# Kernel optimization log

Measured on AMD Instinct MI355X. Metric: run time of the kernel, lower is better.

## Reference

```python
import jax, jax.numpy as jnp
import numpy as np

T = 16          # timesteps
BATCH = 8       # video clips -> leading dim of x is BATCH*T = 128
C_IN = 768      # fixed by nn.Conv2d(768, redu_dim, 1)
D = 256         # redu_dim
K = 64          # num_centers
H = W = 28
EPS = 1e-12     # torch F.normalize eps


def _conv(x, w, padding):
    # x: [N,C,H,W], w: [O,I,kh,kw]
    return jax.lax.conv_general_dilated(
        x, w, window_strides=(1, 1), padding=padding,
        dimension_numbers=('NCHW', 'OIHW', 'NCHW'))


def setup_inputs() -> dict:
    key = jax.random.key(0)
    ks = jax.random.split(key, 9)
    x = jax.random.normal(ks[0], (BATCH * T, C_IN, H, W), dtype=jnp.float32)
    redu_w = jax.random.normal(ks[1], (D, C_IN, 1, 1), jnp.float32) * 0.02
    redu_b = jnp.zeros((D,), jnp.float32)
    share_w = jax.random.normal(ks[2], (K, D, 1, 1), jnp.float32) * 0.05
    share_b = jnp.zeros((K,), jnp.float32)
    U_z = jax.random.normal(ks[3], (K, K, 3, 3), jnp.float32) * 0.04
    U_r = jax.random.normal(ks[4], (K, K, 3, 3), jnp.float32) * 0.04
    U_h = jax.random.normal(ks[5], (K, K, 3, 3), jnp.float32) * 0.04
    centers = jax.random.normal(ks[6], (K, D), jnp.float32) * 0.06
    return {"x": x, "redu_w": redu_w, "redu_b": redu_b,
            "share_w": share_w, "share_b": share_b,
            "U_z": U_z, "U_r": U_r, "U_h": U_h,
            "centers": centers, "timesteps": T}


def reference(x, redu_w, redu_b, share_w, share_b, U_z, U_r, U_h, centers, timesteps):
    t = timesteps
    bt, _, h, w = x.shape
    b = bt // t
    k = share_w.shape[0]
    d = redu_w.shape[0]

    # channel reduction (1x1 conv)
    xr = _conv(x, redu_w, 'VALID') + redu_b[None, :, None, None]        # [bt,d,h,w]
    # shared assignment logits (1x1 conv)
    wxb = _conv(xr, share_w, 'VALID') + share_b[None, :, None, None]     # [bt,k,h,w]
    wxb = wxb.reshape(b, t, k, h, w).transpose(1, 0, 2, 3, 4)            # [t,b,k,h,w]

    # sequential ConvGRU over timesteps
    h0 = jnp.zeros((b, k, h, w), x.dtype)
    def step(h_tm1, w_t):
        z = jax.nn.sigmoid(w_t + _conv(h_tm1, U_z, 'SAME'))
        r = jax.nn.sigmoid(w_t + _conv(h_tm1, U_r, 'SAME'))
        hh = jnp.tanh(w_t + _conv(r * h_tm1, U_h, 'SAME'))
        h_new = (1.0 - z) * hh + z * h_tm1
        return h_new, h_new
    _, hs = jax.lax.scan(step, h0, wxb)                                  # [t,b,k,h,w]

    assign = hs.transpose(1, 0, 2, 3, 4).reshape(b * t, k, h * w)        # [bt,k,hw]
    # softmax over centers per spatial location
    assign = jax.nn.softmax(assign, axis=1)

    # VLAD aggregation
    a_sum = assign.sum(axis=-1, keepdims=True)                           # [bt,k,1]
    a = a_sum * centers[None]                                            # [bt,k,d]
    xf = xr.reshape(b * t, d, h * w)                                     # [bt,d,hw]
    vlad = jnp.einsum('bkp,bdp->bkd', assign, xf) - a                    # [bt,k,d]

    vlad = vlad.reshape(b, t, k, d).sum(axis=1)                          # [b,k,d]
    # intra-norm over feature dim, then global L2 norm
    vlad = vlad / jnp.maximum(jnp.linalg.norm(vlad, axis=2, keepdims=True), EPS)
    vlad = vlad.reshape(b, k * d)
    vlad = vlad / jnp.maximum(jnp.linalg.norm(vlad, axis=1, keepdims=True), EPS)
    return vlad
```

## Files before the change

kernel.cpp:

```cpp
#include <hip/hip_runtime.h>
#include <hip/hip_bf16.h>

#define T_ 16
#define B_ 8
#define CIN 768
#define D_ 256
#define K_ 64
#define HW 784
#define W_ 28

typedef short short8 __attribute__((ext_vector_type(8)));
typedef short short4v __attribute__((ext_vector_type(4)));
typedef float floatx4 __attribute__((ext_vector_type(4)));
typedef unsigned short ushort_t;

__device__ __forceinline__ unsigned short f2bf(float x) {
    union { float f; unsigned u; } v; v.f = x;
    unsigned u = v.u;
    unsigned r = (u + 0x7fffu + ((u >> 16) & 1u)) >> 16;
    return (unsigned short)r;
}
__device__ __forceinline__ float bf2f(unsigned short h) {
    union { unsigned u; float f; } v; v.u = ((unsigned)h) << 16; return v.f;
}

__device__ __forceinline__ float block_reduce_sum_256(float v) {
    for (int off = 32; off > 0; off >>= 1) v += __shfl_down(v, off, 64);
    __shared__ float red[4];
    __shared__ float tot;
    int lane = threadIdx.x & 63, wid = threadIdx.x >> 6;
    if (lane == 0) red[wid] = v;
    __syncthreads();
    if (threadIdx.x == 0) tot = red[0] + red[1] + red[2] + red[3];
    __syncthreads();
    return tot;
}

__global__ __launch_bounds__(256) void cvt_weights(
    const float* __restrict__ rw, const float* __restrict__ sw,
    const float* __restrict__ Uz, const float* __restrict__ Ur,
    const float* __restrict__ Uh,
    ushort_t* __restrict__ whi, ushort_t* __restrict__ wlo,
    ushort_t* __restrict__ shi, ushort_t* __restrict__ slo,
    ushort_t* __restrict__ azh, ushort_t* __restrict__ azl,
    ushort_t* __restrict__ ahh, ushort_t* __restrict__ ahl)
{
    int i = blockIdx.x * 256 + threadIdx.x;
    const int nR = D_ * CIN;
    const int nS = K_ * D_;
    const int nZR = 128 * 576;
    const int nH = 64 * 576;
    if (i < nR) {
        float x = rw[i];
        unsigned short h = f2bf(x);
        whi[i] = h; wlo[i] = f2bf(x - bf2f(h));
    } else if (i < nR + nS) {
        int j = i - nR;
        float x = sw[j];
        unsigned short h = f2bf(x);
        shi[j] = h; slo[j] = f2bf(x - bf2f(h));
    } else if (i < nR + nS + nZR) {
        int j = i - nR - nS;
        int row = j / 576, kk = j - row * 576;
        int tap = kk >> 6, c = kk & 63;
        const float* U = (row < 64) ? Uz : Ur;
        float x = U[(((size_t)(row & 63)) * 64 + c) * 9 + tap];
        unsigned short h = f2bf(x);
        azh[j] = h; azl[j] = f2bf(x - bf2f(h));
    } else if (i < nR + nS + nZR + nH) {
        int j = i - nR - nS - nZR;
        int row = j / 576, kk = j - row * 576;
        int tap = kk >> 6, c = kk & 63;
        float x = Uh[(((size_t)row) * 64 + c) * 9 + tap];
        unsigned short h = f2bf(x);
        ahh[j] = h; ahl[j] = f2bf(x - bf2f(h));
    }
}

template<int BM>
__global__ __launch_bounds__(256, 2) void mfma_conv1x1(
    const float* __restrict__ X, const ushort_t* __restrict__ Whi,
    const ushort_t* __restrict__ Wlo, const float* __restrict__ bias,
    float* __restrict__ Out, int Kdim)
{
    const int nt = blockIdx.x, bt = blockIdx.z;
    const int p0 = nt * 112;
    const int tid = threadIdx.x, lane = tid & 63, wv = tid >> 6;
    const float* Xb = X + (size_t)bt * Kdim * HW;
    float* Ob = Out + (size_t)bt * BM * HW;

    __shared__ ushort_t lA[2][BM * 40];
    __shared__ ushort_t lB[2][112 * 40];

    constexpr int NI = (BM == 256) ? 7 : 2;
    floatx4 acc[4][NI];
#pragma unroll
    for (int a = 0; a < 4; ++a)
#pragma unroll
        for (int b = 0; b < NI; ++b) acc[a][b] = (floatx4){0.f, 0.f, 0.f, 0.f};

    const int NKS = Kdim / 32;
    for (int ks = 0; ks < NKS; ++ks) {
        const int k0 = ks * 32;
#pragma unroll
        for (int i = 0; i < BM / 64; ++i) {
            int ch = tid + i * 256;
            int m = ch >> 2, j = ch & 3;
            uint4 hv = *(const uint4*)(Whi + (size_t)m * Kdim + k0 + j * 8);
            uint4 lv = *(const uint4*)(Wlo + (size_t)m * Kdim + k0 + j * 8);
            *(uint4*)&lA[0][m * 40 + j * 8] = hv;
            *(uint4*)&lA[1][m * 40 + j * 8] = lv;
        }
#pragma unroll
        for (int i = 0; i < 14; ++i) {
            int e = tid + i * 256;
            int cc = e / 112, pp = e - cc * 112;
            float xv = Xb[(size_t)(k0 + cc) * HW + p0 + pp];
            unsigned short h = f2bf(xv);
            lB[0][pp * 40 + cc] = h;
            lB[1][pp * 40 + cc] = f2bf(xv - bf2f(h));
        }
        __syncthreads();

        short8 ahi[4], alo[4];
        const int mbase = (BM == 256) ? wv * 64 : 0;
        const int koff = (lane >> 4) * 8;
#pragma unroll
        for (int mi = 0; mi < 4; ++mi) {
            int m = mbase + mi * 16 + (lane & 15);
            ahi[mi] = *(const short8*)&lA[0][m * 40 + koff];
            alo[mi] = *(const short8*)&lA[1][m * 40 + koff];
        }
        if constexpr (BM == 256) {
#pragma unroll
            for (int ni = 0; ni < 7; ++ni) {
                int n = ni * 16 + (lane & 15);
                short8 bhi = *(const short8*)&lB[0][n * 40 + koff];
                short8 blo = *(const short8*)&lB[1][n * 40 + koff];
#pragma unroll
                for (int mi = 0; mi < 4; ++mi) {
                    acc[mi][ni] = __builtin_amdgcn_mfma_f32_16x16x32_bf16(ahi[mi], bhi, acc[mi][ni], 0, 0, 0);
                    acc[mi][ni] = __builtin_amdgcn_mfma_f32_16x16x32_bf16(ahi[mi], blo, acc[mi][ni], 0, 0, 0);
                    acc[mi][ni] = __builtin_amdgcn_mfma_f32_16x16x32_bf16(alo[mi], bhi, acc[mi][ni], 0, 0, 0);
                }
            }
        } else {
#pragma unroll
            for (int nj = 0; nj < 2; ++nj) {
                int ni = wv * 2 + nj;
                if (ni >= 7) break;
                int n = ni * 16 + (lane & 15);
                short8 bhi = *(const short8*)&lB[0][n * 40 + koff];
                short8 blo = *(const short8*)&lB[1][n * 40 + koff];
#pragma unroll
                for (int mi = 0; mi < 4; ++mi) {
                    acc[mi][nj] = __builtin_amdgcn_mfma_f32_16x16x32_bf16(ahi[mi], bhi, acc[mi][nj], 0, 0, 0);
                    acc[mi][nj] = __builtin_amdgcn_mfma_f32_16x16x32_bf16(ahi[mi], blo, acc[mi][nj], 0, 0, 0);
                    acc[mi][nj] = __builtin_amdgcn_mfma_f32_16x16x32_bf16(alo[mi], bhi, acc[mi][nj], 0, 0, 0);
                }
            }
        }
        __syncthreads();
    }

    if constexpr (BM == 256) {
#pragma unroll
        for (int mi = 0; mi < 4; ++mi) {
            int m0g = wv * 64 + mi * 16 + ((lane >> 4) << 2);
#pragma unroll
            for (int ni = 0; ni < 7; ++ni) {
                int p = p0 + ni * 16 + (lane & 15);
#pragma unroll
                for (int r = 0; r < 4; ++r)
                    Ob[(size_t)(m0g + r) * HW + p] = acc[mi][ni][r] + bias[m0g + r];
            }
        }
    } else {
#pragma unroll
        for (int nj = 0; nj < 2; ++nj) {
            int ni = wv * 2 + nj;
            if (ni >= 7) break;
            int p = p0 + ni * 16 + (lane & 15);
#pragma unroll
            for (int mi = 0; mi < 4; ++mi) {
                int m0g = mi * 16 + ((lane >> 4) << 2);
#pragma unroll
                for (int r = 0; r < 4; ++r)
                    Ob[(size_t)(m0g + r) * HW + p] = acc[mi][nj][r] + bias[m0g + r];
            }
        }
    }
}

__device__ __forceinline__ void stage_tile(
    const ushort_t* __restrict__ ghi, const ushort_t* __restrict__ glo,
    ushort_t* Bhi, ushort_t* Blo, int y0, int tid)
{
    for (int e = tid; e < 6 * 30 * 8; e += 256) {
        int r = e / 240, rem = e - r * 240;
        int lx = rem >> 3, j = rem & 7;
        int gy = y0 - 1 + r, gx = lx - 1;
        short8 vh = {0, 0, 0, 0, 0, 0, 0, 0};
        short8 vl = {0, 0, 0, 0, 0, 0, 0, 0};
        if (gy >= 0 && gy < 28 && gx >= 0 && gx < 28) {
            size_t go = ((size_t)(gy * 28 + gx)) * 64 + j * 8;
            vh = *(const short8*)(ghi + go);
            vl = *(const short8*)(glo + go);
        }
        int lo = (r * 30 + lx) * 72 + j * 8;
        *(short8*)&Bhi[lo] = vh;
        *(short8*)&Blo[lo] = vl;
    }
}

__device__ __forceinline__ void gru_gemm(
    const ushort_t* __restrict__ Ahi, const ushort_t* __restrict__ Alo,
    int arow, int Astride,
    const ushort_t* Bhi, const ushort_t* Blo, int lane, floatx4 acc[7])
{
    const int koff8 = (lane >> 4) * 8;
    const int li = lane & 15;
    int yb[7], xb[7];
#pragma unroll
    for (int nf = 0; nf < 7; ++nf) {
        int pp = nf * 16 + li;
        yb[nf] = pp / 28; xb[nf] = pp - yb[nf] * 28;
    }
    for (int tap = 0; tap < 9; ++tap) {
        int dy = tap / 3, dx = tap - dy * 3;
#pragma unroll
        for (int ch = 0; ch < 2; ++ch) {
            int kk = tap * 64 + ch * 32 + koff8;
            short8 ahi = *(const short8*)(Ahi + (size_t)arow * Astride + kk);
            short8 alo = *(const short8*)(Alo + (size_t)arow * Astride + kk);
            int cbase = ch * 32 + koff8;
#pragma unroll
            for (int nf = 0; nf < 7; ++nf) {
                int o = ((yb[nf] + dy) * 30 + xb[nf] + dx) * 72 + cbase;
                short8 bhi = *(const short8*)&Bhi[o];
                short8 blo = *(const short8*)&Blo[o];
                acc[nf] = __builtin_amdgcn_mfma_f32_16x16x32_bf16(ahi, bhi, acc[nf], 0, 0, 0);
                acc[nf] = __builtin_amdgcn_mfma_f32_16x16x32_bf16(ahi, blo, acc[nf], 0, 0, 0);
                acc[nf] = __builtin_amdgcn_mfma_f32_16x16x32_bf16(alo, bhi, acc[nf], 0, 0, 0);
            }
        }
    }
}

__global__ __launch_bounds__(256, 2) void gru_zr_mfma(
    const ushort_t* __restrict__ hhi, const ushort_t* __restrict__ hlo,
    const ushort_t* __restrict__ azh, const ushort_t* __restrict__ azl,
    const float* __restrict__ wxb, const float* __restrict__ hprev_f,
    float* __restrict__ zbuf, ushort_t* __restrict__ rhi, ushort_t* __restrict__ rlo,
    int t)
{
    int rt = blockIdx.x, b = blockIdx.y, half = blockIdx.z;
    int y0 = rt * 4;
    int tid = threadIdx.x, lane = tid & 63, wv = tid >> 6;

    __shared__ ushort_t Bhi[6 * 30 * 72];
    __shared__ ushort_t Blo[6 * 30 * 72];
    stage_tile(hhi + (size_t)b * HW * 64, hlo + (size_t)b * HW * 64, Bhi, Blo, y0, tid);
    __syncthreads();

    floatx4 acc[7];
#pragma unroll
    for (int nf = 0; nf < 7; ++nf) acc[nf] = (floatx4){0.f, 0.f, 0.f, 0.f};

    int arow = half * 64 + wv * 16 + (lane & 15);
    gru_gemm(azh, azl, arow, 576, Bhi, Blo, lane, acc);

    int kbase = wv * 16 + ((lane >> 4) << 2);
    const float* wx = wxb + (((size_t)b * T_ + t) * K_) * HW;
    const float* hp = hprev_f + (size_t)b * K_ * HW;
#pragma unroll
    for (int nf = 0; nf < 7; ++nf) {
        int p = y0 * 28 + nf * 16 + (lane & 15);
        if (half == 0) {
#pragma unroll
            for (int r = 0; r < 4; ++r) {
                int k = kbase + r;
                float g = 1.f / (1.f + __expf(-(wx[(size_t)k * HW + p] + acc[nf][r])));
                zbuf[((size_t)b * K_ + k) * HW + p] = g;
            }
        } else {
            short4v vh, vl;
#pragma unroll
            for (int r = 0; r < 4; ++r) {
                int k = kbase + r;
                float g = 1.f / (1.f + __expf(-(wx[(size_t)k * HW + p] + acc[nf][r])));
                float rh = g * hp[(size_t)k * HW + p];
                unsigned short h = f2bf(rh);
                vh[r] = h; vl[r] = f2bf(rh - bf2f(h));
            }
            size_t o = (size_t)(b * HW + p) * 64 + kbase;
            *(short4v*)(rhi + o) = vh;
            *(short4v*)(rlo + o) = vl;
        }
    }
}

__global__ __launch_bounds__(256, 2) void gru_h_mfma(
    const ushort_t* __restrict__ rhi, const ushort_t* __restrict__ rlo,
    const ushort_t* __restrict__ ahh, const ushort_t* __restrict__ ahl,
    const float* __restrict__ wxb, const float* __restrict__ hprev_f,
    const float* __restrict__ zbuf, float* __restrict__ hs_t,
    ushort_t* __restrict__ hhi, ushort_t* __restrict__ hlo, int t)
{
    int rt = blockIdx.x, b = blockIdx.y;
    int y0 = rt * 4;
    int tid = threadIdx.x, lane = tid & 63, wv = tid >> 6;

    __shared__ ushort_t Bhi[6 * 30 * 72];
    __shared__ ushort_t Blo[6 * 30 * 72];
    stage_tile(rhi + (size_t)b * HW * 64, rlo + (size_t)b * HW * 64, Bhi, Blo, y0, tid);
    __syncthreads();

    floatx4 acc[7];
#pragma unroll
    for (int nf = 0; nf < 7; ++nf) acc[nf] = (floatx4){0.f, 0.f, 0.f, 0.f};

    int arow = wv * 16 + (lane & 15);
    gru_gemm(ahh, ahl, arow, 576, Bhi, Blo, lane, acc);

    int kbase = wv * 16 + ((lane >> 4) << 2);
    const float* wx = wxb + (((size_t)b * T_ + t) * K_) * HW;
    const float* hp = hprev_f + (size_t)b * K_ * HW;
#pragma unroll
    for (int nf = 0; nf < 7; ++nf) {
        int p = y0 * 28 + nf * 16 + (lane & 15);
        short4v vh, vl;
#pragma unroll
        for (int r = 0; r < 4; ++r) {
            int k = kbase + r;
            float xv = wx[(size_t)k * HW + p] + acc[nf][r];
            float e2 = __expf(2.f * xv);
            float th = 1.f - 2.f / (e2 + 1.f);
            float z = zbuf[((size_t)b * K_ + k) * HW + p];
            float hpv = hp[(size_t)k * HW + p];
            float hn = (1.f - z) * th + z * hpv;
            hs_t[((size_t)b * K_ + k) * HW + p] = hn;
            unsigned short h = f2bf(hn);
            vh[r] = h; vl[r] = f2bf(hn - bf2f(h));
        }
        size_t o = (size_t)(b * HW + p) * 64 + kbase;
        *(short4v*)(hhi + o) = vh;
        *(short4v*)(hlo + o) = vl;
    }
}

__global__ __launch_bounds__(256) void softmax_k(float* __restrict__ hs)
{
    int q = blockIdx.x;
    float* base = hs + (size_t)q * K_ * HW;
    for (int p = threadIdx.x; p < HW; p += 256) {
        float v[64];
        float m = -1e30f;
#pragma unroll
        for (int k = 0; k < 64; ++k) {
            v[k] = base[(size_t)k * HW + p];
            m = fmaxf(m, v[k]);
        }
        float s = 0.f;
#pragma unroll
        for (int k = 0; k < 64; ++k) {
            v[k] = __expf(v[k] - m);
            s += v[k];
        }
        float inv = 1.f / s;
#pragma unroll
        for (int k = 0; k < 64; ++k)
            base[(size_t)k * HW + p] = v[k] * inv;
    }
}

__global__ __launch_bounds__(256) void asum_k(const float* __restrict__ hs,
                                              float* __restrict__ asum)
{
    int bid = blockIdx.x; int b = bid >> 6, k = bid & 63;
    float s = 0.f;
    for (int t = 0; t < T_; ++t) {
        const float* row = hs + (((size_t)t * B_ + b) * K_ + k) * HW;
        for (int p = threadIdx.x; p < HW; p += 256) s += row[p];
    }
    float tot = block_reduce_sum_256(s);
    if (threadIdx.x == 0) asum[bid] = tot;
}

__global__ __launch_bounds__(256) void vlad_k(const float* __restrict__ assign,
    const float* __restrict__ xr, float* __restrict__ vladt)
{
    int dt = blockIdx.x, t = blockIdx.y, b = blockIdx.z;
    int q = t * B_ + b, bt = b * T_ + t, d0 = dt * 64;
    const float* ab = assign + (size_t)q * K_ * HW;
    const float* xb = xr + (size_t)bt * D_ * HW;
    __shared__ float As[16][68];
    __shared__ float Xs[16][68];
    int tx = threadIdx.x & 15, ty = threadIdx.x >> 4;
    float acc[4][4] = {{0.f}};

    for (int p0 = 0; p0 < HW; p0 += 16) {
#pragma unroll
        for (int it = 0; it < 4; ++it) {
            int e = threadIdx.x + it * 256;
            int row = e >> 4, pp = e & 15;
            As[pp][row] = ab[(size_t)row * HW + p0 + pp];
            Xs[pp][row] = xb[(size_t)(d0 + row) * HW + p0 + pp];
        }
        __syncthreads();
#pragma unroll
        for (int pp = 0; pp < 16; ++pp) {
            float4 a = *(const float4*)&As[pp][ty * 4];
            float4 xv = *(const float4*)&Xs[pp][tx * 4];
            float av[4] = {a.x, a.y, a.z, a.w};
            float xvv[4] = {xv.x, xv.y, xv.z, xv.w};
#pragma unroll
            for (int r = 0; r < 4; ++r)
#pragma unroll
                for (int s = 0; s < 4; ++s)
                    acc[r][s] = fmaf(av[r], xvv[s], acc[r][s]);
        }
        __syncthreads();
    }
#pragma unroll
    for (int r = 0; r < 4; ++r) {
        int k = ty * 4 + r;
        float4 o = {acc[r][0], acc[r][1], acc[r][2], acc[r][3]};
        *(float4*)&vladt[((size_t)bt * K_ + k) * D_ + d0 + tx * 4] = o;
    }
}

__global__ __launch_bounds__(256) void norm1_k(const float* __restrict__ vladt,
    const float* __restrict__ asum, const float* __restrict__ centers,
    float* __restrict__ out)
{
    int bid = blockIdx.x; int b = bid >> 6, k = bid & 63; int d = threadIdx.x;
    float acc = 0.f;
#pragma unroll
    for (int t = 0; t < T_; ++t)
        acc += vladt[(((size_t)b * T_ + t) * K_ + k) * D_ + d];
    acc -= asum[bid] * centers[(size_t)k * D_ + d];
    float ss = block_reduce_sum_256(acc * acc);
    float n = fmaxf(sqrtf(ss), 1e-12f);
    out[((size_t)b * K_ + k) * D_ + d] = acc / n;
}

__global__ __launch_bounds__(256) void norm2_k(float* __restrict__ out)
{
    int b = blockIdx.x;
    float* v = out + (size_t)b * (K_ * D_);
    float s = 0.f;
    for (int i = threadIdx.x; i < K_ * D_; i += 256) {
        float x = v[i];
        s = fmaf(x, x, s);
    }
    float tot = block_reduce_sum_256(s);
    float n = fmaxf(sqrtf(tot), 1e-12f);
    for (int i = threadIdx.x; i < K_ * D_; i += 256) v[i] = v[i] / n;
}

extern "C" void kernel_launch(void* const* d_in, const int* in_sizes, int n_in,
                              void* d_out, int out_size, void* d_ws, size_t ws_size,
                              hipStream_t stream)
{
    const float* x       = (const float*)d_in[0];
    const float* redu_w  = (const float*)d_in[1];
    const float* redu_b  = (const float*)d_in[2];
    const float* share_w = (const float*)d_in[3];
    const float* share_b = (const float*)d_in[4];
    const float* Uz      = (const float*)d_in[5];
    const float* Ur      = (const float*)d_in[6];
    const float* Uh      = (const float*)d_in[7];
    const float* centers = (const float*)d_in[8];

    float* ws = (float*)d_ws;
    const size_t SZ_XR   = (size_t)128 * D_ * HW;
    const size_t SZ_WXB  = (size_t)128 * K_ * HW;
    const size_t SZ_HS   = (size_t)T_ * B_ * K_ * HW;
    const size_t SZ_PLANE= (size_t)B_ * K_ * HW;

    float* xr    = ws;
    float* wxb   = xr + SZ_XR;
    float* hs    = wxb + SZ_WXB;
    float* h0    = hs + SZ_HS;
    float* zbuf  = h0 + SZ_PLANE;
    float* asumb = zbuf + SZ_PLANE;
    float* wsplit= asumb + 512;
    float* area  = wsplit + 323584;

    ushort_t* whi = (ushort_t*)wsplit;
    ushort_t* wlo = whi + 196608;
    ushort_t* shi = wlo + 196608;
    ushort_t* slo = shi + 16384;
    ushort_t* azh = slo + 16384;
    ushort_t* azl = azh + 73728;
    ushort_t* ahh = azl + 73728;
    ushort_t* ahl = ahh + 36864;

    float* vladt = area;
    ushort_t* hhi = (ushort_t*)area;
    ushort_t* hlo = hhi + SZ_PLANE;
    ushort_t* rhi = hlo + SZ_PLANE;
    ushort_t* rlo = rhi + SZ_PLANE;

    hipMemsetAsync(h0, 0, SZ_PLANE * sizeof(float), stream);
    hipMemsetAsync(hhi, 0, 2 * SZ_PLANE * sizeof(ushort_t), stream);

    cvt_weights<<<dim3((D_ * CIN + K_ * D_ + 128 * 576 + 64 * 576 + 255) / 256),
                  256, 0, stream>>>(redu_w, share_w, Uz, Ur, Uh,
                                    whi, wlo, shi, slo, azh, azl, ahh, ahl);

    mfma_conv1x1<256><<<dim3(7, 1, 128), 256, 0, stream>>>(x, whi, wlo, redu_b, xr, CIN);
    mfma_conv1x1<64><<<dim3(7, 1, 128), 256, 0, stream>>>(xr, shi, slo, share_b, wxb, D_);

    for (int t = 0; t < T_; ++t) {
        const float* hp = (t == 0) ? h0 : hs + (size_t)(t - 1) * SZ_PLANE;
        gru_zr_mfma<<<dim3(7, 8, 2), 256, 0, stream>>>(hhi, hlo, azh, azl, wxb, hp,
                                                       zbuf, rhi, rlo, t);
        gru_h_mfma<<<dim3(7, 8), 256, 0, stream>>>(rhi, rlo, ahh, ahl, wxb, hp, zbuf,
                                                   hs + (size_t)t * SZ_PLANE, hhi, hlo, t);
    }

    softmax_k<<<128, 256, 0, stream>>>(hs);
    asum_k<<<512, 256, 0, stream>>>(hs, asumb);

    vlad_k<<<dim3(4, 16, 8), 256, 0, stream>>>(hs, xr, vladt);
    norm1_k<<<512, 256, 0, stream>>>(vladt, asumb, centers, (float*)d_out);
    norm2_k<<<8, 256, 0, stream>>>((float*)d_out);
}
```

Before: 795.5 us.

## Fuse GRU gate kernels per step, pipeline conv1x1 loads, split softmax grid

```diff
diff --git a/kernel.cpp b/kernel.cpp
--- a/kernel.cpp
+++ b/kernel.cpp
@@ -77,64 +77,81 @@
     }
 }
 
-template<int BM>
+template<int BM, int KD>
 __global__ __launch_bounds__(256, 2) void mfma_conv1x1(
     const float* __restrict__ X, const ushort_t* __restrict__ Whi,
     const ushort_t* __restrict__ Wlo, const float* __restrict__ bias,
-    float* __restrict__ Out, int Kdim)
+    float* __restrict__ Out)
 {
     const int nt = blockIdx.x, bt = blockIdx.z;
     const int p0 = nt * 112;
     const int tid = threadIdx.x, lane = tid & 63, wv = tid >> 6;
-    const float* Xb = X + (size_t)bt * Kdim * HW;
+    const float* Xb = X + (size_t)bt * KD * HW;
     float* Ob = Out + (size_t)bt * BM * HW;
 
-    __shared__ ushort_t lA[2][BM * 40];
     __shared__ ushort_t lB[2][112 * 40];
 
     constexpr int NI = (BM == 256) ? 7 : 2;
+    constexpr int NKS = KD / 32;
     floatx4 acc[4][NI];
 #pragma unroll
     for (int a = 0; a < 4; ++a)
 #pragma unroll
         for (int b = 0; b < NI; ++b) acc[a][b] = (floatx4){0.f, 0.f, 0.f, 0.f};
 
-    const int NKS = Kdim / 32;
-    for (int ks = 0; ks < NKS; ++ks) {
-        const int k0 = ks * 32;
-#pragma unroll
-        for (int i = 0; i < BM / 64; ++i) {
-            int ch = tid + i * 256;
-            int m = ch >> 2, j = ch & 3;
-            uint4 hv = *(const uint4*)(Whi + (size_t)m * Kdim + k0 + j * 8);
-            uint4 lv = *(const uint4*)(Wlo + (size_t)m * Kdim + k0 + j * 8);
-            *(uint4*)&lA[0][m * 40 + j * 8] = hv;
-            *(uint4*)&lA[1][m * 40 + j * 8] = lv;
-        }
-#pragma unroll
-        for (int i = 0; i < 14; ++i) {
-            int e = tid + i * 256;
-            int cc = e / 112, pp = e - cc * 112;
-            float xv = Xb[(size_t)(k0 + cc) * HW + p0 + pp];
-            unsigned short h = f2bf(xv);
-            lB[0][pp * 40 + cc] = h;
-            lB[1][pp * 40 + cc] = f2bf(xv - bf2f(h));
-        }
-        __syncthreads();
-
-        short8 ahi[4], alo[4];
-        const int mbase = (BM == 256) ? wv * 64 : 0;
-        const int koff = (lane >> 4) * 8;
+    const int koff = (lane >> 4) * 8;
+    const int li = lane & 15;
+    const int mbase = (BM == 256) ? wv * 64 : 0;
+
+    const int u0j = tid / 112, u0p = tid - u0j * 112;
+    const bool u1v = tid < 192;
+    const int u1j = (tid + 256) / 112, u1p = (tid + 256) - u1j * 112;
+
+    float b0[16], b1[16];
+    short8 ahi[4], alo[4];
+
+    auto loadB = [&](int k0, float* bb) {
+        const float* xp0 = Xb + (size_t)(k0 + u0j * 8) * HW + p0 + u0p;
+#pragma unroll
+        for (int c = 0; c < 8; ++c) bb[c] = xp0[c * HW];
+        if (u1v) {
+            const float* xp1 = Xb + (size_t)(k0 + u1j * 8) * HW + p0 + u1p;
+#pragma unroll
+            for (int c = 0; c < 8; ++c) bb[8 + c] = xp1[c * HW];
+        }
+    };
+    auto writeB = [&](const float* bb) {
+        short8 vh, vl;
+#pragma unroll
+        for (int c = 0; c < 8; ++c) {
+            unsigned short h = f2bf(bb[c]);
+            vh[c] = (short)h; vl[c] = (short)f2bf(bb[c] - bf2f(h));
+        }
+        *(short8*)&lB[0][u0p * 40 + u0j * 8] = vh;
+        *(short8*)&lB[1][u0p * 40 + u0j * 8] = vl;
+        if (u1v) {
+#pragma unroll
+            for (int c = 0; c < 8; ++c) {
+                unsigned short h = f2bf(bb[8 + c]);
+                vh[c] = (short)h; vl[c] = (short)f2bf(bb[8 + c] - bf2f(h));
+            }
+            *(short8*)&lB[0][u1p * 40 + u1j * 8] = vh;
+            *(short8*)&lB[1][u1p * 40 + u1j * 8] = vl;
+        }
+    };
+    auto loadA = [&](int k0) {
 #pragma unroll
         for (int mi = 0; mi < 4; ++mi) {
-            int m = mbase + mi * 16 + (lane & 15);
-            ahi[mi] = *(const short8*)&lA[0][m * 40 + koff];
-            alo[mi] = *(const short8*)&lA[1][m * 40 + koff];
-        }
+            int m = mbase + mi * 16 + li;
+            ahi[mi] = *(const short8*)(Whi + (size_t)m * KD + k0 + koff);
+            alo[mi] = *(const short8*)(Wlo + (size_t)m * KD + k0 + koff);
+        }
+    };
+    auto domfma = [&]() {
         if constexpr (BM == 256) {
 #pragma unroll
             for (int ni = 0; ni < 7; ++ni) {
-                int n = ni * 16 + (lane & 15);
+                int n = ni * 16 + li;
                 short8 bhi = *(const short8*)&lB[0][n * 40 + koff];
                 short8 blo = *(const short8*)&lB[1][n * 40 + koff];
 #pragma unroll
@@ -149,7 +166,7 @@
             for (int nj = 0; nj < 2; ++nj) {
                 int ni = wv * 2 + nj;
                 if (ni >= 7) break;
-                int n = ni * 16 + (lane & 15);
+                int n = ni * 16 + li;
                 short8 bhi = *(const short8*)&lB[0][n * 40 + koff];
                 short8 blo = *(const short8*)&lB[1][n * 40 + koff];
 #pragma unroll
@@ -160,6 +177,21 @@
                 }
             }
         }
+    };
+
+    loadB(0, b0);
+    for (int ks = 0; ks < NKS; ks += 2) {
+        loadA(ks * 32);
+        writeB(b0);
+        __syncthreads();
+        if (ks + 1 < NKS) loadB((ks + 1) * 32, b1);
+        domfma();
+        __syncthreads();
+        loadA((ks + 1) * 32);
+        writeB(b1);
+        __syncthreads();
+        if (ks + 2 < NKS) loadB((ks + 2) * 32, b0);
+        domfma();
         __syncthreads();
     }
 
@@ -169,7 +201,7 @@
             int m0g = wv * 64 + mi * 16 + ((lane >> 4) << 2);
 #pragma unroll
             for (int ni = 0; ni < 7; ++ni) {
-                int p = p0 + ni * 16 + (lane & 15);
+                int p = p0 + ni * 16 + li;
 #pragma unroll
                 for (int r = 0; r < 4; ++r)
                     Ob[(size_t)(m0g + r) * HW + p] = acc[mi][ni][r] + bias[m0g + r];
@@ -180,7 +212,7 @@
         for (int nj = 0; nj < 2; ++nj) {
             int ni = wv * 2 + nj;
             if (ni >= 7) break;
-            int p = p0 + ni * 16 + (lane & 15);
+            int p = p0 + ni * 16 + li;
 #pragma unroll
             for (int mi = 0; mi < 4; ++mi) {
                 int m0g = mi * 16 + ((lane >> 4) << 2);
@@ -192,168 +224,216 @@
     }
 }
 
-__device__ __forceinline__ void stage_tile(
-    const ushort_t* __restrict__ ghi, const ushort_t* __restrict__ glo,
-    ushort_t* Bhi, ushort_t* Blo, int y0, int tid)
-{
-    for (int e = tid; e < 6 * 30 * 8; e += 256) {
-        int r = e / 240, rem = e - r * 240;
-        int lx = rem >> 3, j = rem & 7;
-        int gy = y0 - 1 + r, gx = lx - 1;
-        short8 vh = {0, 0, 0, 0, 0, 0, 0, 0};
-        short8 vl = {0, 0, 0, 0, 0, 0, 0, 0};
-        if (gy >= 0 && gy < 28 && gx >= 0 && gx < 28) {
-            size_t go = ((size_t)(gy * 28 + gx)) * 64 + j * 8;
-            vh = *(const short8*)(ghi + go);
-            vl = *(const short8*)(glo + go);
-        }
-        int lo = (r * 30 + lx) * 72 + j * 8;
-        *(short8*)&Bhi[lo] = vh;
-        *(short8*)&Blo[lo] = vl;
-    }
-}
-
-__device__ __forceinline__ void gru_gemm(
-    const ushort_t* __restrict__ Ahi, const ushort_t* __restrict__ Alo,
-    int arow, int Astride,
-    const ushort_t* Bhi, const ushort_t* Blo, int lane, floatx4 acc[7])
-{
-    const int koff8 = (lane >> 4) * 8;
-    const int li = lane & 15;
-    int yb[7], xb[7];
-#pragma unroll
-    for (int nf = 0; nf < 7; ++nf) {
-        int pp = nf * 16 + li;
-        yb[nf] = pp / 28; xb[nf] = pp - yb[nf] * 28;
-    }
-    for (int tap = 0; tap < 9; ++tap) {
-        int dy = tap / 3, dx = tap - dy * 3;
-#pragma unroll
-        for (int ch = 0; ch < 2; ++ch) {
-            int kk = tap * 64 + ch * 32 + koff8;
-            short8 ahi = *(const short8*)(Ahi + (size_t)arow * Astride + kk);
-            short8 alo = *(const short8*)(Alo + (size_t)arow * Astride + kk);
-            int cbase = ch * 32 + koff8;
-#pragma unroll
-            for (int nf = 0; nf < 7; ++nf) {
-                int o = ((yb[nf] + dy) * 30 + xb[nf] + dx) * 72 + cbase;
-                short8 bhi = *(const short8*)&Bhi[o];
-                short8 blo = *(const short8*)&Blo[o];
-                acc[nf] = __builtin_amdgcn_mfma_f32_16x16x32_bf16(ahi, bhi, acc[nf], 0, 0, 0);
-                acc[nf] = __builtin_amdgcn_mfma_f32_16x16x32_bf16(ahi, blo, acc[nf], 0, 0, 0);
-                acc[nf] = __builtin_amdgcn_mfma_f32_16x16x32_bf16(alo, bhi, acc[nf], 0, 0, 0);
-            }
-        }
-    }
-}
-
-__global__ __launch_bounds__(256, 2) void gru_zr_mfma(
-    const ushort_t* __restrict__ hhi, const ushort_t* __restrict__ hlo,
+__global__ __launch_bounds__(512, 2) void gru_step(
+    const ushort_t* __restrict__ hRhi, const ushort_t* __restrict__ hRlo,
+    ushort_t* __restrict__ hWhi, ushort_t* __restrict__ hWlo,
     const ushort_t* __restrict__ azh, const ushort_t* __restrict__ azl,
-    const float* __restrict__ wxb, const float* __restrict__ hprev_f,
-    float* __restrict__ zbuf, ushort_t* __restrict__ rhi, ushort_t* __restrict__ rlo,
-    int t)
-{
-    int rt = blockIdx.x, b = blockIdx.y, half = blockIdx.z;
-    int y0 = rt * 4;
-    int tid = threadIdx.x, lane = tid & 63, wv = tid >> 6;
-
-    __shared__ ushort_t Bhi[6 * 30 * 72];
-    __shared__ ushort_t Blo[6 * 30 * 72];
-    stage_tile(hhi + (size_t)b * HW * 64, hlo + (size_t)b * HW * 64, Bhi, Blo, y0, tid);
+    const ushort_t* __restrict__ ahh, const ushort_t* __restrict__ ahl,
+    const float* __restrict__ wxb, float* __restrict__ hs_t, int t)
+{
+    const int y0 = blockIdx.x, b = blockIdx.y;
+    const int tid = threadIdx.x, lane = tid & 63, wv = tid >> 6;
+    const int li = lane & 15, koff8 = (lane >> 4) * 8, kq = (lane >> 4) * 4;
+
+    __shared__ ushort_t Hhi[5 * 30 * 72], Hlo[5 * 30 * 72];
+    __shared__ ushort_t Rhi[3 * 30 * 72], Rlo[3 * 30 * 72];
+    __shared__ float zs[28 * 68];
+
+    {
+        const ushort_t* gh = hRhi + (size_t)b * HW * 64;
+        const ushort_t* gl = hRlo + (size_t)b * HW * 64;
+        for (int e = tid; e < 1200; e += 512) {
+            int r = e / 240, rem = e - r * 240;
+            int lx = rem >> 3, j = rem & 7;
+            int gy = y0 - 2 + r, gx = lx - 1;
+            short8 vh = {0,0,0,0,0,0,0,0}, vl = {0,0,0,0,0,0,0,0};
+            if (gy >= 0 && gy < 28 && gx >= 0 && gx < 28) {
+                size_t go = ((size_t)(gy * 28 + gx)) * 64 + j * 8;
+                vh = *(const short8*)(gh + go);
+                vl = *(const short8*)(gl + go);
+            }
+            int lo = (r * 30 + lx) * 72 + j * 8;
+            *(short8*)&Hhi[lo] = vh;
+            *(short8*)&Hlo[lo] = vl;
+        }
+        short8 z8 = {0,0,0,0,0,0,0,0};
+        for (int e = tid; e < 1620; e += 512) {
+            if (e < 810) *(short8*)&Rhi[e * 8] = z8;
+            else         *(short8*)&Rlo[(e - 810) * 8] = z8;
+        }
+    }
     __syncthreads();
 
-    floatx4 acc[7];
-#pragma unroll
-    for (int nf = 0; nf < 7; ++nf) acc[nf] = (floatx4){0.f, 0.f, 0.f, 0.f};
-
-    int arow = half * 64 + wv * 16 + (lane & 15);
-    gru_gemm(azh, azl, arow, 576, Bhi, Blo, lane, acc);
-
-    int kbase = wv * 16 + ((lane >> 4) << 2);
-    const float* wx = wxb + (((size_t)b * T_ + t) * K_) * HW;
-    const float* hp = hprev_f + (size_t)b * K_ * HW;
-#pragma unroll
-    for (int nf = 0; nf < 7; ++nf) {
-        int p = y0 * 28 + nf * 16 + (lane & 15);
-        if (half == 0) {
+    const float* wx = wxb + ((size_t)(b * T_ + t) * K_) * HW;
+    const int c0 = li;
+    const int c1 = (li < 12) ? 16 + li : 0;
+
+    if (wv < 4) {
+        const int kb = wv * 16;
+        const ushort_t* Ah = azh + (size_t)(kb + li) * 576;
+        const ushort_t* Al = azl + (size_t)(kb + li) * 576;
+        floatx4 az[2];
+        az[0] = (floatx4){0.f,0.f,0.f,0.f}; az[1] = (floatx4){0.f,0.f,0.f,0.f};
+#pragma unroll
+        for (int tap = 0; tap < 9; ++tap) {
+            const int dy = tap / 3, dx = tap - dy * 3;
+#pragma unroll
+            for (int ch = 0; ch < 2; ++ch) {
+                short8 whi_ = *(const short8*)(Ah + tap * 64 + ch * 32 + koff8);
+                short8 wlo_ = *(const short8*)(Al + tap * 64 + ch * 32 + koff8);
+                int cb = ch * 32 + koff8;
+                int o0 = ((dy + 1) * 30 + c0 + dx) * 72 + cb;
+                int o1 = ((dy + 1) * 30 + c1 + dx) * 72 + cb;
+                short8 bh0 = *(const short8*)&Hhi[o0];
+                short8 bl0 = *(const short8*)&Hlo[o0];
+                short8 bh1 = *(const short8*)&Hhi[o1];
+                short8 bl1 = *(const short8*)&Hlo[o1];
+                az[0] = __builtin_amdgcn_mfma_f32_16x16x32_bf16(whi_, bh0, az[0], 0, 0, 0);
+                az[0] = __builtin_amdgcn_mfma_f32_16x16x32_bf16(whi_, bl0, az[0], 0, 0, 0);
+                az[0] = __builtin_amdgcn_mfma_f32_16x16x32_bf16(wlo_, bh0, az[0], 0, 0, 0);
+                az[1] = __builtin_amdgcn_mfma_f32_16x16x32_bf16(whi_, bh1, az[1], 0, 0, 0);
+                az[1] = __builtin_amdgcn_mfma_f32_16x16x32_bf16(whi_, bl1, az[1], 0, 0, 0);
+                az[1] = __builtin_amdgcn_mfma_f32_16x16x32_bf16(wlo_, bh1, az[1], 0, 0, 0);
+            }
+        }
+        const int kb4 = kb + kq;
+#pragma unroll
+        for (int cf = 0; cf < 2; ++cf) {
+            int c = cf * 16 + li;
+            if (c < 28) {
+                floatx4 zv;
+#pragma unroll
+                for (int r = 0; r < 4; ++r)
+                    zv[r] = 1.f / (1.f + __expf(-(wx[(size_t)(kb4 + r) * HW + y0 * 28 + c] + az[cf][r])));
+                *(floatx4*)&zs[c * 68 + kb4] = zv;
+            }
+        }
+    } else {
+        const int kb = (wv - 4) * 16;
+        const ushort_t* Ah = azh + (size_t)(64 + kb + li) * 576;
+        const ushort_t* Al = azl + (size_t)(64 + kb + li) * 576;
+        floatx4 ar[3][2];
+#pragma unroll
+        for (int i = 0; i < 3; ++i) {
+            ar[i][0] = (floatx4){0.f,0.f,0.f,0.f};
+            ar[i][1] = (floatx4){0.f,0.f,0.f,0.f};
+        }
+#pragma unroll
+        for (int tap = 0; tap < 9; ++tap) {
+            const int dy = tap / 3, dx = tap - dy * 3;
+#pragma unroll
+            for (int ch = 0; ch < 2; ++ch) {
+                short8 whi_ = *(const short8*)(Ah + tap * 64 + ch * 32 + koff8);
+                short8 wlo_ = *(const short8*)(Al + tap * 64 + ch * 32 + koff8);
+                int cb = ch * 32 + koff8;
+#pragma unroll
+                for (int rr = 0; rr < 3; ++rr) {
+                    int o0 = ((rr + dy) * 30 + c0 + dx) * 72 + cb;
+                    int o1 = ((rr + dy) * 30 + c1 + dx) * 72 + cb;
+                    short8 bh0 = *(const short8*)&Hhi[o0];
+                    short8 bl0 = *(const short8*)&Hlo[o0];
+                    short8 bh1 = *(const short8*)&Hhi[o1];
+                    short8 bl1 = *(const short8*)&Hlo[o1];
+                    ar[rr][0] = __builtin_amdgcn_mfma_f32_16x16x32_bf16(whi_, bh0, ar[rr][0], 0, 0, 0);
+                    ar[rr][0] = __builtin_amdgcn_mfma_f32_16x16x32_bf16(whi_, bl0, ar[rr][0], 0, 0, 0);
+                    ar[rr][0] = __builtin_amdgcn_mfma_f32_16x16x32_bf16(wlo_, bh0, ar[rr][0], 0, 0, 0);
+                    ar[rr][1] = __builtin_amdgcn_mfma_f32_16x16x32_bf16(whi_, bh1, ar[rr][1], 0, 0, 0);
+                    ar[rr][1] = __builtin_amdgcn_mfma_f32_16x16x32_bf16(whi_, bl1, ar[rr][1], 0, 0, 0);
+                    ar[rr][1] = __builtin_amdgcn_mfma_f32_16x16x32_bf16(wlo_, bh1, ar[rr][1], 0, 0, 0);
+                }
+            }
+        }
+        const int kb4 = kb + kq;
+#pragma unroll
+        for (int rr = 0; rr < 3; ++rr) {
+            int gy = y0 - 1 + rr;
+            if (gy < 0 || gy >= 28) continue;
+#pragma unroll
+            for (int cf = 0; cf < 2; ++cf) {
+                int c = cf * 16 + li;
+                if (c >= 28) continue;
+                short4v ph = *(const short4v*)&Hhi[((rr + 1) * 30 + c + 1) * 72 + kb4];
+                short4v pl = *(const short4v*)&Hlo[((rr + 1) * 30 + c + 1) * 72 + kb4];
+                short4v vh, vl;
+#pragma unroll
+                for (int r = 0; r < 4; ++r) {
+                    float rv = 1.f / (1.f + __expf(-(wx[(size_t)(kb4 + r) * HW + gy * 28 + c] + ar[rr][cf][r])));
+                    float hv = bf2f((unsigned short)ph[r]) + bf2f((unsigned short)pl[r]);
+                    float rh = rv * hv;
+                    unsigned short h = f2bf(rh);
+                    vh[r] = (short)h; vl[r] = (short)f2bf(rh - bf2f(h));
+                }
+                *(short4v*)&Rhi[(rr * 30 + c + 1) * 72 + kb4] = vh;
+                *(short4v*)&Rlo[(rr * 30 + c + 1) * 72 + kb4] = vl;
+            }
+        }
+    }
+    __syncthreads();
+
+    if (wv < 4) {
+        const int kb = wv * 16;
+        const ushort_t* Ah = ahh + (size_t)(kb + li) * 576;
+        const ushort_t* Al = ahl + (size_t)(kb + li) * 576;
+        floatx4 ac[2];
+        ac[0] = (floatx4){0.f,0.f,0.f,0.f}; ac[1] = (floatx4){0.f,0.f,0.f,0.f};
+#pragma unroll
+        for (int tap = 0; tap < 9; ++tap) {
+            const int dy = tap / 3, dx = tap - dy * 3;
+#pragma unroll
+            for (int ch = 0; ch < 2; ++ch) {
+                short8 whi_ = *(const short8*)(Ah + tap * 64 + ch * 32 + koff8);
+                short8 wlo_ = *(const short8*)(Al + tap * 64 + ch * 32 + koff8);
+                int cb = ch * 32 + koff8;
+                int o0 = (dy * 30 + c0 + dx) * 72 + cb;
+                int o1 = (dy * 30 + c1 + dx) * 72 + cb;
+                short8 bh0 = *(const short8*)&Rhi[o0];
+                short8 bl0 = *(const short8*)&Rlo[o0];
+                short8 bh1 = *(const short8*)&Rhi[o1];
+                short8 bl1 = *(const short8*)&Rlo[o1];
+                ac[0] = __builtin_amdgcn_mfma_f32_16x16x32_bf16(whi_, bh0, ac[0], 0, 0, 0);
+                ac[0] = __builtin_amdgcn_mfma_f32_16x16x32_bf16(whi_, bl0, ac[0], 0, 0, 0);
+                ac[0] = __builtin_amdgcn_mfma_f32_16x16x32_bf16(wlo_, bh0, ac[0], 0, 0, 0);
+                ac[1] = __builtin_amdgcn_mfma_f32_16x16x32_bf16(whi_, bh1, ac[1], 0, 0, 0);
+                ac[1] = __builtin_amdgcn_mfma_f32_16x16x32_bf16(whi_, bl1, ac[1], 0, 0, 0);
+                ac[1] = __builtin_amdgcn_mfma_f32_16x16x32_bf16(wlo_, bh1, ac[1], 0, 0, 0);
+            }
+        }
+        const int kb4 = kb + kq;
+        float* hsb = hs_t + (size_t)b * K_ * HW;
+#pragma unroll
+        for (int cf = 0; cf < 2; ++cf) {
+            int c = cf * 16 + li;
+            if (c >= 28) continue;
+            int p = y0 * 28 + c;
+            floatx4 zv = *(const floatx4*)&zs[c * 68 + kb4];
+            short4v ph = *(const short4v*)&Hhi[(2 * 30 + c + 1) * 72 + kb4];
+            short4v pl = *(const short4v*)&Hlo[(2 * 30 + c + 1) * 72 + kb4];
+            short4v vh, vl;
 #pragma unroll
             for (int r = 0; r < 4; ++r) {
-                int k = kbase + r;
-                float g = 1.f / (1.f + __expf(-(wx[(size_t)k * HW + p] + acc[nf][r])));
-                zbuf[((size_t)b * K_ + k) * HW + p] = g;
-            }
-        } else {
-            short4v vh, vl;
-#pragma unroll
-            for (int r = 0; r < 4; ++r) {
-                int k = kbase + r;
-                float g = 1.f / (1.f + __expf(-(wx[(size_t)k * HW + p] + acc[nf][r])));
-                float rh = g * hp[(size_t)k * HW + p];
-                unsigned short h = f2bf(rh);
-                vh[r] = h; vl[r] = f2bf(rh - bf2f(h));
-            }
-            size_t o = (size_t)(b * HW + p) * 64 + kbase;
-            *(short4v*)(rhi + o) = vh;
-            *(short4v*)(rlo + o) = vl;
-        }
-    }
-}
-
-__global__ __launch_bounds__(256, 2) void gru_h_mfma(
-    const ushort_t* __restrict__ rhi, const ushort_t* __restrict__ rlo,
-    const ushort_t* __restrict__ ahh, const ushort_t* __restrict__ ahl,
-    const float* __restrict__ wxb, const float* __restrict__ hprev_f,
-    const float* __restrict__ zbuf, float* __restrict__ hs_t,
-    ushort_t* __restrict__ hhi, ushort_t* __restrict__ hlo, int t)
-{
-    int rt = blockIdx.x, b = blockIdx.y;
-    int y0 = rt * 4;
-    int tid = threadIdx.x, lane = tid & 63, wv = tid >> 6;
-
-    __shared__ ushort_t Bhi[6 * 30 * 72];
-    __shared__ ushort_t Blo[6 * 30 * 72];
-    stage_tile(rhi + (size_t)b * HW * 64, rlo + (size_t)b * HW * 64, Bhi, Blo, y0, tid);
-    __syncthreads();
-
-    floatx4 acc[7];
-#pragma unroll
-    for (int nf = 0; nf < 7; ++nf) acc[nf] = (floatx4){0.f, 0.f, 0.f, 0.f};
-
-    int arow = wv * 16 + (lane & 15);
-    gru_gemm(ahh, ahl, arow, 576, Bhi, Blo, lane, acc);
-
-    int kbase = wv * 16 + ((lane >> 4) << 2);
-    const float* wx = wxb + (((size_t)b * T_ + t) * K_) * HW;
-    const float* hp = hprev_f + (size_t)b * K_ * HW;
-#pragma unroll
-    for (int nf = 0; nf < 7; ++nf) {
-        int p = y0 * 28 + nf * 16 + (lane & 15);
-        short4v vh, vl;
-#pragma unroll
-        for (int r = 0; r < 4; ++r) {
-            int k = kbase + r;
-            float xv = wx[(size_t)k * HW + p] + acc[nf][r];
-            float e2 = __expf(2.f * xv);
-            float th = 1.f - 2.f / (e2 + 1.f);
-            float z = zbuf[((size_t)b * K_ + k) * HW + p];
-            float hpv = hp[(size_t)k * HW + p];
-            float hn = (1.f - z) * th + z * hpv;
-            hs_t[((size_t)b * K_ + k) * HW + p] = hn;
-            unsigned short h = f2bf(hn);
-            vh[r] = h; vl[r] = f2bf(hn - bf2f(h));
-        }
-        size_t o = (size_t)(b * HW + p) * 64 + kbase;
-        *(short4v*)(hhi + o) = vh;
-        *(short4v*)(hlo + o) = vl;
+                int k = kb4 + r;
+                float xv = wx[(size_t)k * HW + p] + ac[cf][r];
+                float e2 = __expf(2.f * xv);
+                float th = 1.f - 2.f / (e2 + 1.f);
+                float hp = bf2f((unsigned short)ph[r]) + bf2f((unsigned short)pl[r]);
+                float hn = (1.f - zv[r]) * th + zv[r] * hp;
+                hsb[(size_t)k * HW + p] = hn;
+                unsigned short h = f2bf(hn);
+                vh[r] = (short)h; vl[r] = (short)f2bf(hn - bf2f(h));
+            }
+            size_t o = ((size_t)(b * HW) + p) * 64 + kb4;
+            *(short4v*)(hWhi + o) = vh;
+            *(short4v*)(hWlo + o) = vl;
+        }
     }
 }
 
 __global__ __launch_bounds__(256) void softmax_k(float* __restrict__ hs)
 {
     int q = blockIdx.x;
+    int py = blockIdx.y;
     float* base = hs + (size_t)q * K_ * HW;
-    for (int p = threadIdx.x; p < HW; p += 256) {
+    for (int p = py * 392 + threadIdx.x; p < (py + 1) * 392 && p < HW; p += 256) {
         float v[64];
         float m = -1e30f;
 #pragma unroll
@@ -482,9 +562,7 @@
     float* xr    = ws;
     float* wxb   = xr + SZ_XR;
     float* hs    = wxb + SZ_WXB;
-    float* h0    = hs + SZ_HS;
-    float* zbuf  = h0 + SZ_PLANE;
-    float* asumb = zbuf + SZ_PLANE;
+    float* asumb = hs + SZ_HS;
     float* wsplit= asumb + 512;
     float* area  = wsplit + 323584;
 
@@ -498,30 +576,32 @@
     ushort_t* ahl = ahh + 36864;
 
     float* vladt = area;
-    ushort_t* hhi = (ushort_t*)area;
-    ushort_t* hlo = hhi + SZ_PLANE;
-    ushort_t* rhi = hlo + SZ_PLANE;
-    ushort_t* rlo = rhi + SZ_PLANE;
-
-    hipMemsetAsync(h0, 0, SZ_PLANE * sizeof(float), stream);
-    hipMemsetAsync(hhi, 0, 2 * SZ_PLANE * sizeof(ushort_t), stream);
+    ushort_t* st = (ushort_t*)area;
+    ushort_t* h0hi = st;
+    ushort_t* h0lo = st + SZ_PLANE;
+    ushort_t* h1hi = st + 2 * SZ_PLANE;
+    ushort_t* h1lo = st + 3 * SZ_PLANE;
+
+    hipMemsetAsync(h0hi, 0, 2 * SZ_PLANE * sizeof(ushort_t), stream);
 
     cvt_weights<<<dim3((D_ * CIN + K_ * D_ + 128 * 576 + 64 * 576 + 255) / 256),
                   256, 0, stream>>>(redu_w, share_w, Uz, Ur, Uh,
                                     whi, wlo, shi, slo, azh, azl, ahh, ahl);
 
-    mfma_conv1x1<256><<<dim3(7, 1, 128), 256, 0, stream>>>(x, whi, wlo, redu_b, xr, CIN);
-    mfma_conv1x1<64><<<dim3(7, 1, 128), 256, 0, stream>>>(xr, shi, slo, share_b, wxb, D_);
+    mfma_conv1x1<256, CIN><<<dim3(7, 1, 128), 256, 0, stream>>>(x, whi, wlo, redu_b, xr);
+    mfma_conv1x1<64, D_><<<dim3(7, 1, 128), 256, 0, stream>>>(xr, shi, slo, share_b, wxb);
 
     for (int t = 0; t < T_; ++t) {
-        const float* hp = (t == 0) ? h0 : hs + (size_t)(t - 1) * SZ_PLANE;
-        gru_zr_mfma<<<dim3(7, 8, 2), 256, 0, stream>>>(hhi, hlo, azh, azl, wxb, hp,
-                                                       zbuf, rhi, rlo, t);
-        gru_h_mfma<<<dim3(7, 8), 256, 0, stream>>>(rhi, rlo, ahh, ahl, wxb, hp, zbuf,
-                                                   hs + (size_t)t * SZ_PLANE, hhi, hlo, t);
-    }
-
-    softmax_k<<<128, 256, 0, stream>>>(hs);
+        const ushort_t* rh_ = (t & 1) ? h1hi : h0hi;
+        const ushort_t* rl_ = (t & 1) ? h1lo : h0lo;
+        ushort_t* wh_ = (t & 1) ? h0hi : h1hi;
+        ushort_t* wl_ = (t & 1) ? h0lo : h1lo;
+        gru_step<<<dim3(28, 8), 512, 0, stream>>>(rh_, rl_, wh_, wl_,
+                                                  azh, azl, ahh, ahl,
+                                                  wxb, hs + (size_t)t * SZ_PLANE, t);
+    }
+
+    softmax_k<<<dim3(128, 2), 256, 0, stream>>>(hs);
     asum_k<<<512, 256, 0, stream>>>(hs, asumb);
 
     vlad_k<<<dim3(4, 16, 8), 256, 0, stream>>>(hs, xr, vladt);
```

Measured after the change: 674.2 us. -15.3%, faster.
